# Optimization experiments

Hardware: AMD Instinct MI355X
Metric: run time of the kernel (lower is better)

## Reference

```python
import jax, jax.numpy as jnp
import numpy as np

E = 20000       # num edges (nodes of the edge-adjacency graph)
FDIM = 128      # edge_feature_dim
D = 16          # stalk_dim ('diagonal' => mlp output dim = D)
P = 300000      # number of adjacent (i, j) pairs extracted from L1
EPS = 1e-5      # LayerNorm eps


def _xavier(key, fan_in, fan_out):
    lim = np.sqrt(6.0 / (fan_in + fan_out)).astype(np.float32)
    return jax.random.uniform(key, (fan_in, fan_out), jnp.float32, -lim, lim)


def _layernorm(x, g, b):
    mu = jnp.mean(x, axis=-1, keepdims=True)
    var = jnp.mean((x - mu) ** 2, axis=-1, keepdims=True)
    return (x - mu) * jax.lax.rsqrt(var + EPS) * g + b


def setup_inputs() -> dict:
    key = jax.random.key(0)
    ks = jax.random.split(key, 8)
    return {
        "edge_features": jax.random.normal(ks[0], (E, FDIM), jnp.float32),
        "pair_i": jax.random.randint(ks[1], (P,), 0, E),
        "pair_j": jax.random.randint(ks[2], (P,), 0, E),
        # MLP: Linear(2F,64) -> LN -> ReLU -> Linear(64,32) -> LN -> ReLU -> Linear(32,D)
        "W1": _xavier(ks[3], 2 * FDIM, 64), "b1": jnp.zeros((64,), jnp.float32),
        "g1": jnp.ones((64,), jnp.float32), "be1": jnp.zeros((64,), jnp.float32),
        "W2": _xavier(ks[4], 64, 32), "b2": jnp.zeros((32,), jnp.float32),
        "g2": jnp.ones((32,), jnp.float32), "be2": jnp.zeros((32,), jnp.float32),
        "W3": _xavier(ks[5], 32, D), "b3": jnp.zeros((D,), jnp.float32),
    }


def reference(edge_features, pair_i, pair_j, W1, b1, g1, be1, W2, b2, g2, be2, W3, b3):
    # Gather the two edge feature vectors per adjacent pair and concat: [P, 2F]
    x = jnp.concatenate([edge_features[pair_i], edge_features[pair_j]], axis=1)
    h = jax.nn.relu(_layernorm(x @ W1 + b1, g1, be1))      # [P, 64]
    h = jax.nn.relu(_layernorm(h @ W2 + b2, g2, be2))      # [P, 32]
    params = h @ W3 + b3                                    # [P, D]
    # diagonal sheaf: F_ij = diag(params) for every pair, batched (diag_embed)
    return params[:, :, None] * jnp.eye(D, dtype=params.dtype)  # [P, D, D]
```

## Files before the change

### kernel.cpp

```cpp
#include <hip/hip_runtime.h>

typedef float f32x4 __attribute__((ext_vector_type(4)));

__global__ void bad_map_marker(float* out) {
    if (threadIdx.x == 0 && blockIdx.x == 0) out[0] = 1.0e6f;
}

__device__ __forceinline__ void mlp_tail_compute(float* h, float* pr, int D,
        const float* __restrict__ g1, const float* __restrict__ be1,
        const float* __restrict__ W2, const float* __restrict__ b2,
        const float* __restrict__ g2, const float* __restrict__ be2,
        const float* __restrict__ W3, const float* __restrict__ b3) {
    float s = 0.f, ss = 0.f;
    #pragma unroll
    for (int d = 0; d < 64; ++d) { s += h[d]; ss += h[d] * h[d]; }
    float mu  = s * (1.f / 64.f);
    float inv = rsqrtf(ss * (1.f / 64.f) - mu * mu + 1e-5f);
    #pragma unroll
    for (int d = 0; d < 64; ++d)
        h[d] = fmaxf((h[d] - mu) * inv * g1[d] + be1[d], 0.f);

    float a2[32];
    const float4* w2v = (const float4*)W2;
    #pragma unroll
    for (int n = 0; n < 32; ++n) a2[n] = b2[n];
    for (int k = 0; k < 64; ++k) {
        float hk = h[k];
        #pragma unroll
        for (int q = 0; q < 8; ++q) {
            float4 w = w2v[k * 8 + q];
            a2[4 * q + 0] += hk * w.x;
            a2[4 * q + 1] += hk * w.y;
            a2[4 * q + 2] += hk * w.z;
            a2[4 * q + 3] += hk * w.w;
        }
    }
    s = 0.f; ss = 0.f;
    #pragma unroll
    for (int n = 0; n < 32; ++n) { s += a2[n]; ss += a2[n] * a2[n]; }
    mu  = s * (1.f / 32.f);
    inv = rsqrtf(ss * (1.f / 32.f) - mu * mu + 1e-5f);
    #pragma unroll
    for (int n = 0; n < 32; ++n)
        a2[n] = fmaxf((a2[n] - mu) * inv * g2[n] + be2[n], 0.f);

    for (int d = 0; d < D; ++d) pr[d] = b3[d];
    for (int k = 0; k < 32; ++k) {
        float hk = a2[k];
        const float* wr = W3 + k * D;
        for (int d = 0; d < D; ++d) pr[d] += hk * wr[d];
    }
}

__device__ __forceinline__ void store_diag16_f32_256(const float* pp, float* out, int P) {
    const int t = threadIdx.x;
    f32x4* outv = (f32x4*)out + (size_t)blockIdx.x * 16384;
    const int pbase = blockIdx.x * 256;
    #pragma unroll 8
    for (int it = 0; it < 64; ++it) {
        int g = it * 256 + t;
        int pl = g >> 6;
        int rem = g & 63;
        int d = rem >> 2;
        int c4 = rem & 3;
        float val = pp[pl * 17 + d];
        bool on = (d >> 2) == c4;
        f32x4 v;
        v.x = (on && (d & 3) == 0) ? val : 0.f;
        v.y = (on && (d & 3) == 1) ? val : 0.f;
        v.z = (on && (d & 3) == 2) ? val : 0.f;
        v.w = (on && (d & 3) == 3) ? val : 0.f;
        if (pbase + pl < P) __builtin_nontemporal_store(v, &outv[g]);
    }
}

__global__ __launch_bounds__(256)
void precompute_y(const float* __restrict__ ef, const float* __restrict__ W1,
                  const float* __restrict__ b1, float* __restrict__ Y, int E) {
    __shared__ __align__(16) float el[16 * 132];
    const int t = threadIdx.x;
    const int ebase = blockIdx.x * 16;

    for (int idx = t; idx < 512; idx += 256) {
        int er = idx >> 5, ec = idx & 31;
        if (ebase + er < E)
            *((float4*)(el + er * 132) + ec) =
                *((const float4*)(ef + (size_t)(ebase + er) * 128) + ec);
    }
    __syncthreads();

    const int eg  = t & 15;
    const int cgi = t >> 4;
    const int half  = cgi >> 3;
    const int col64 = (cgi & 7) * 8;

    float acc[8];
    #pragma unroll
    for (int c = 0; c < 8; ++c) acc[c] = 0.f;

    const float* wbase = W1 + (size_t)half * 128 * 64 + col64;
    const float* erow  = el + eg * 132;
    #pragma unroll 4
    for (int k = 0; k < 128; ++k) {
        float4 w0 = *(const float4*)(wbase + (size_t)k * 64);
        float4 w1 = *(const float4*)(wbase + (size_t)k * 64 + 4);
        float a = erow[k];
        acc[0] += a * w0.x; acc[1] += a * w0.y;
        acc[2] += a * w0.z; acc[3] += a * w0.w;
        acc[4] += a * w1.x; acc[5] += a * w1.y;
        acc[6] += a * w1.z; acc[7] += a * w1.w;
    }

    #pragma unroll
    for (int c = 0; c < 8; ++c) acc[c] += (half == 0) ? b1[col64 + c] : 0.f;

    int e = ebase + eg;
    if (e < E) {
        float* dst = Y + (size_t)e * 128 + half * 64 + col64;
        *(float4*)(dst)     = make_float4(acc[0], acc[1], acc[2], acc[3]);
        *(float4*)(dst + 4) = make_float4(acc[4], acc[5], acc[6], acc[7]);
    }
}

__global__ __launch_bounds__(256)
void sheaf_pairs(const int* __restrict__ pi, const int* __restrict__ pj,
                 const float* __restrict__ Y,
                 const float* __restrict__ g1, const float* __restrict__ be1,
                 const float* __restrict__ W2, const float* __restrict__ b2,
                 const float* __restrict__ g2, const float* __restrict__ be2,
                 const float* __restrict__ W3, const float* __restrict__ b3,
                 float* __restrict__ out, int P) {
    __shared__ float pp[256 * 17];
    int p = blockIdx.x * 256 + threadIdx.x;
    int pc = p < P ? p : P - 1;
    int i = pi[pc], j = pj[pc];
    const float4* y1 = (const float4*)(Y + (size_t)i * 128);
    const float4* y2 = (const float4*)(Y + (size_t)j * 128 + 64);
    float h[64];
    #pragma unroll
    for (int q = 0; q < 16; ++q) {
        float4 a = y1[q], b = y2[q];
        h[4 * q + 0] = a.x + b.x;
        h[4 * q + 1] = a.y + b.y;
        h[4 * q + 2] = a.z + b.z;
        h[4 * q + 3] = a.w + b.w;
    }
    float pr[16];
    mlp_tail_compute(h, pr, 16, g1, be1, W2, b2, g2, be2, W3, b3);
    #pragma unroll
    for (int d = 0; d < 16; ++d) pp[threadIdx.x * 17 + d] = pr[d];
    __syncthreads();
    store_diag16_f32_256(pp, out, P);
}

__global__ __launch_bounds__(256)
void sheaf_generic(const float* __restrict__ ef,
                   const int* __restrict__ pi, const int* __restrict__ pj,
                   const float* __restrict__ W1, const float* __restrict__ b1,
                   const float* __restrict__ g1, const float* __restrict__ be1,
                   const float* __restrict__ W2, const float* __restrict__ b2,
                   const float* __restrict__ g2, const float* __restrict__ be2,
                   const float* __restrict__ W3, const float* __restrict__ b3,
                   float* __restrict__ out, int P, int F, int D) {
    __shared__ float pp[256 * 17];
    int p = blockIdx.x * 256 + threadIdx.x;
    int pc = p < P ? p : P - 1;
    int i = pi[pc], j = pj[pc];
    const float* efi = ef + (size_t)i * F;
    const float* efj = ef + (size_t)j * F;
    float h[64];
    #pragma unroll
    for (int n = 0; n < 64; ++n) h[n] = b1[n];
    for (int k = 0; k < F; ++k) {
        float ei = efi[k];
        float ej = efj[k];
        const float* wi = W1 + (size_t)k * 64;
        const float* wj = W1 + (size_t)(F + k) * 64;
        #pragma unroll
        for (int n = 0; n < 64; ++n) h[n] += ei * wi[n] + ej * wj[n];
    }
    float pr[32];
    mlp_tail_compute(h, pr, D, g1, be1, W2, b2, g2, be2, W3, b3);

    if (D == 16) {
        #pragma unroll
        for (int d = 0; d < 16; ++d) pp[threadIdx.x * 17 + d] = pr[d];
        __syncthreads();
        store_diag16_f32_256(pp, out, P);
    } else {
        if (p < P) {
            float* po = out + (size_t)p * D * D;
            for (int r = 0; r < D; ++r) {
                float dv = pr[r];
                for (int c = 0; c < D; ++c)
                    __builtin_nontemporal_store((r == c) ? dv : 0.f, &po[r * D + c]);
            }
        }
    }
}

struct Map { int ef, pi, pj, w1, b1, g1, be1, w2, b2, g2, be2, w3, b3; };

static bool validate_map(const Map& m, const int* s, int n_in, long out_size,
                         int* Fo, int* Eo, int* Do, int* Po) {
    if (n_in < 13) return false;
    if (s[m.b1] != 64 || s[m.g1] != 64 || s[m.be1] != 64) return false;
    if (s[m.b2] != 32 || s[m.g2] != 32 || s[m.be2] != 32) return false;
    if (s[m.w2] != 64 * 32) return false;
    long w1 = s[m.w1];
    if (w1 <= 0 || (w1 % 128) != 0) return false;
    long F = w1 / 128;
    if (F <= 0) return false;
    int D = s[m.b3];
    if (D <= 0 || D > 32) return false;
    if (s[m.w3] != 32 * D) return false;
    long P = s[m.pi];
    if (P <= 0 || s[m.pj] != P) return false;
    long ef = s[m.ef];
    if (ef <= 0 || (ef % F) != 0) return false;
    long E = ef / F;
    if (out_size != P * D * D) return false;
    *Fo = (int)F; *Eo = (int)E; *Do = D; *Po = (int)P;
    return true;
}

extern "C" void kernel_launch(void* const* d_in, const int* in_sizes, int n_in,
                              void* d_out, int out_size, void* d_ws, size_t ws_size,
                              hipStream_t stream) {
    const Map pos   = {0, 1, 2, 3, 4, 5, 6, 7, 8, 9, 10, 11, 12};
    const Map alpha = {8, 11, 12, 0, 3, 9, 6, 1, 4, 10, 7, 2, 5};

    int F = 0, E = 0, D = 0, P = 0;
    Map m;
    if (validate_map(pos, in_sizes, n_in, (long)out_size, &F, &E, &D, &P)) {
        m = pos;
    } else if (validate_map(alpha, in_sizes, n_in, (long)out_size, &F, &E, &D, &P)) {
        m = alpha;
    } else {
        bad_map_marker<<<dim3(1), dim3(64), 0, stream>>>((float*)d_out);
        return;
    }

    const float* ef  = (const float*)d_in[m.ef];
    const int*   pi  = (const int*)d_in[m.pi];
    const int*   pj  = (const int*)d_in[m.pj];
    const float* W1  = (const float*)d_in[m.w1];
    const float* b1  = (const float*)d_in[m.b1];
    const float* g1  = (const float*)d_in[m.g1];
    const float* be1 = (const float*)d_in[m.be1];
    const float* W2  = (const float*)d_in[m.w2];
    const float* b2  = (const float*)d_in[m.b2];
    const float* g2  = (const float*)d_in[m.g2];
    const float* be2 = (const float*)d_in[m.be2];
    const float* W3  = (const float*)d_in[m.w3];
    const float* b3  = (const float*)d_in[m.b3];
    float* out = (float*)d_out;

    const size_t y_bytes = (size_t)E * 128 * 4;

    if (F == 128 && D == 16 && ws_size >= y_bytes) {
        float* Y = (float*)d_ws;
        precompute_y<<<dim3((E + 15) / 16), dim3(256), 0, stream>>>(ef, W1, b1, Y, E);
        sheaf_pairs<<<dim3((P + 255) / 256), dim3(256), 0, stream>>>(
            pi, pj, Y, g1, be1, W2, b2, g2, be2, W3, b3, out, P);
    } else {
        sheaf_generic<<<dim3((P + 255) / 256), dim3(256), 0, stream>>>(
            ef, pi, pj, W1, b1, g1, be1, W2, b2, g2, be2, W3, b3, out, P, F, D);
    }
}
```

Before: 409.5 us.

## Split pair MLP and diagonal expansion into separate kernels via workspace

Instead of having each pair block compute the MLP and then write its 256x16x16 diagonal output, the pair kernel writes compact 16-float params to workspace and a separate grid-stride kernel expands them into the dense diagonal output. The goal is to decouple the latency-bound gather/compute phase from the bandwidth-bound output store so the store can run at full occupancy. Nontemporal stores are also replaced with plain stores in the remaining paths. The split costs an extra kernel launch and a small params round-trip through memory, and it only runs when the workspace is large enough.

```diff
diff --git a/kernel.cpp b/kernel.cpp
--- a/kernel.cpp
+++ b/kernel.cpp
@@ -54,7 +54,7 @@
 
 __device__ __forceinline__ void store_diag16_f32_256(const float* pp, float* out, int P) {
     const int t = threadIdx.x;
-    f32x4* outv = (f32x4*)out + (size_t)blockIdx.x * 16384;
+    float4* outv = (float4*)out + (size_t)blockIdx.x * 16384;
     const int pbase = blockIdx.x * 256;
     #pragma unroll 8
     for (int it = 0; it < 64; ++it) {
@@ -65,12 +65,12 @@
         int c4 = rem & 3;
         float val = pp[pl * 17 + d];
         bool on = (d >> 2) == c4;
-        f32x4 v;
+        float4 v;
         v.x = (on && (d & 3) == 0) ? val : 0.f;
         v.y = (on && (d & 3) == 1) ? val : 0.f;
         v.z = (on && (d & 3) == 2) ? val : 0.f;
         v.w = (on && (d & 3) == 3) ? val : 0.f;
-        if (pbase + pl < P) __builtin_nontemporal_store(v, &outv[g]);
+        if (pbase + pl < P) outv[g] = v;
     }
 }
 
@@ -119,6 +119,71 @@
         float* dst = Y + (size_t)e * 128 + half * 64 + col64;
         *(float4*)(dst)     = make_float4(acc[0], acc[1], acc[2], acc[3]);
         *(float4*)(dst + 4) = make_float4(acc[4], acc[5], acc[6], acc[7]);
+    }
+}
+
+__global__ __launch_bounds__(256)
+void pairs_params(const int* __restrict__ pi, const int* __restrict__ pj,
+                  const float* __restrict__ Y,
+                  const float* __restrict__ g1, const float* __restrict__ be1,
+                  const float* __restrict__ W2, const float* __restrict__ b2,
+                  const float* __restrict__ g2, const float* __restrict__ be2,
+                  const float* __restrict__ W3, const float* __restrict__ b3,
+                  float* __restrict__ params, int P) {
+    __shared__ float pp[256 * 17];
+    const int t = threadIdx.x;
+    int p = blockIdx.x * 256 + t;
+    int pc = p < P ? p : P - 1;
+    int i = pi[pc], j = pj[pc];
+    const float4* y1 = (const float4*)(Y + (size_t)i * 128);
+    const float4* y2 = (const float4*)(Y + (size_t)j * 128 + 64);
+    float h[64];
+    #pragma unroll
+    for (int q = 0; q < 16; ++q) {
+        float4 a = y1[q], b = y2[q];
+        h[4 * q + 0] = a.x + b.x;
+        h[4 * q + 1] = a.y + b.y;
+        h[4 * q + 2] = a.z + b.z;
+        h[4 * q + 3] = a.w + b.w;
+    }
+    float pr[16];
+    mlp_tail_compute(h, pr, 16, g1, be1, W2, b2, g2, be2, W3, b3);
+    #pragma unroll
+    for (int d = 0; d < 16; ++d) pp[t * 17 + d] = pr[d];
+    __syncthreads();
+
+    float4* pv = (float4*)params + (size_t)blockIdx.x * 1024;
+    const int pbase = blockIdx.x * 256;
+    #pragma unroll
+    for (int it = 0; it < 4; ++it) {
+        int c = it * 256 + t;
+        int pl = c >> 2;
+        int q  = c & 3;
+        const float* src = pp + pl * 17 + q * 4;
+        float4 v = make_float4(src[0], src[1], src[2], src[3]);
+        if (pbase + pl < P) pv[c] = v;
+    }
+}
+
+__global__ __launch_bounds__(256)
+void diag_expand(const float* __restrict__ params, float* __restrict__ out,
+                 long total4) {
+    f32x4* outv = (f32x4*)out;
+    const size_t stride = (size_t)gridDim.x * 256;
+    for (size_t g = (size_t)blockIdx.x * 256 + threadIdx.x; g < (size_t)total4;
+         g += stride) {
+        int pl  = (int)(g >> 6);
+        int rem = (int)(g & 63);
+        int d   = rem >> 2;
+        int c4  = rem & 3;
+        float val = params[(size_t)pl * 16 + d];
+        bool on = (d >> 2) == c4;
+        f32x4 v;
+        v.x = (on && (d & 3) == 0) ? val : 0.f;
+        v.y = (on && (d & 3) == 1) ? val : 0.f;
+        v.z = (on && (d & 3) == 2) ? val : 0.f;
+        v.w = (on && (d & 3) == 3) ? val : 0.f;
+        outv[g] = v;
     }
 }
 
@@ -192,8 +257,7 @@
             float* po = out + (size_t)p * D * D;
             for (int r = 0; r < D; ++r) {
                 float dv = pr[r];
-                for (int c = 0; c < D; ++c)
-                    __builtin_nontemporal_store((r == c) ? dv : 0.f, &po[r * D + c]);
+                for (int c = 0; c < D; ++c) po[r * D + c] = (r == c) ? dv : 0.f;
             }
         }
     }
@@ -257,12 +321,22 @@
     float* out = (float*)d_out;
 
     const size_t y_bytes = (size_t)E * 128 * 4;
+    const size_t p_bytes = (size_t)P * 16 * 4;
 
     if (F == 128 && D == 16 && ws_size >= y_bytes) {
         float* Y = (float*)d_ws;
         precompute_y<<<dim3((E + 15) / 16), dim3(256), 0, stream>>>(ef, W1, b1, Y, E);
-        sheaf_pairs<<<dim3((P + 255) / 256), dim3(256), 0, stream>>>(
-            pi, pj, Y, g1, be1, W2, b2, g2, be2, W3, b3, out, P);
+        if (ws_size >= y_bytes + p_bytes) {
+            float* params = (float*)((char*)d_ws + y_bytes);
+            pairs_params<<<dim3((P + 255) / 256), dim3(256), 0, stream>>>(
+                pi, pj, Y, g1, be1, W2, b2, g2, be2, W3, b3, params, P);
+            long total4 = (long)P * 64;
+            int blocks = 3072;
+            diag_expand<<<dim3(blocks), dim3(256), 0, stream>>>(params, out, total4);
+        } else {
+            sheaf_pairs<<<dim3((P + 255) / 256), dim3(256), 0, stream>>>(
+                pi, pj, Y, g1, be1, W2, b2, g2, be2, W3, b3, out, P);
+        }
     } else {
         sheaf_generic<<<dim3((P + 255) / 256), dim3(256), 0, stream>>>(
             ef, pi, pj, W1, b1, g1, be1, W2, b2, g2, be2, W3, b3, out, P, F, D);
```

Result: slower. 440.8 us (+7.6%).
